# Performance work log

Measured on AMD Instinct MI355X. Metric: run time of the kernel, lower is better.

## Reference

```python
import jax, jax.numpy as jnp
import numpy as np

A = 32      # num_agents (nodes per batch element)
B = 256     # batch size
T = 5       # temporal_window_size
H, C = 4, 64  # attention heads, hidden_dim per head
D = H * C   # feature_dim = 256
NEG_SLOPE = 0.2
LATENT = 128
NBS = 64    # num_belief_states
FIN = NBS + 16  # node_feat_dim = num_belief_states + action_dim


def _xavier(k, shape):
    std = (2.0 / (shape[0] + shape[-1])) ** 0.5
    return std * jax.random.normal(k, shape, dtype=jnp.float32)


def setup_inputs() -> dict:
    key = jax.random.key(0)
    ks = jax.random.split(key, 24)
    N = B * A
    # fully-connected directed graph (no self loops) inside each batch block
    ii, jj = np.meshgrid(np.arange(A), np.arange(A), indexing='ij')
    m = ii != jj
    off = (np.arange(B) * A)[:, None]
    src = (off + ii[m][None, :]).ravel()
    dst = (off + jj[m][None, :]).ravel()
    edge_index = jnp.asarray(np.stack([src, dst]), dtype=jnp.int32)  # [2, E]
    return dict(
        x_seq=jax.random.normal(ks[0], (T, N, FIN), dtype=jnp.float32),
        edge_index=edge_index,
        W1=_xavier(ks[1], (D, FIN)),
        att_src1=0.1 * jax.random.normal(ks[2], (H, C), dtype=jnp.float32),
        att_dst1=0.1 * jax.random.normal(ks[3], (H, C), dtype=jnp.float32),
        b1=jnp.zeros((D,), jnp.float32),
        W2=_xavier(ks[4], (D, D)),
        att_src2=0.1 * jax.random.normal(ks[5], (H, C), dtype=jnp.float32),
        att_dst2=0.1 * jax.random.normal(ks[6], (H, C), dtype=jnp.float32),
        b2=jnp.zeros((D,), jnp.float32),
        in_proj_w=_xavier(ks[7], (3 * D, D)),
        in_proj_b=jnp.zeros((3 * D,), jnp.float32),
        out_proj_w=_xavier(ks[8], (D, D)),
        out_proj_b=jnp.zeros((D,), jnp.float32),
        w_mean=_xavier(ks[9], (LATENT, D)),
        b_mean=jnp.zeros((LATENT,), jnp.float32),
        w_logvar=_xavier(ks[10], (LATENT, D)),
        b_logvar=jnp.zeros((LATENT,), jnp.float32),
        w_belief=_xavier(ks[11], (NBS, D)),
        b_belief=jnp.zeros((NBS,), jnp.float32),
    )


def _gat(x, src, dst, W, a_src, a_dst, bias, N):
    """PyG-style GATConv (concat heads, self loops already in src/dst, eval mode)."""
    h = (x @ W.T).reshape(N, H, C)                         # [N,H,C]
    e = (h * a_src).sum(-1)[src] + (h * a_dst).sum(-1)[dst]  # [E,H]
    e = jax.nn.leaky_relu(e, NEG_SLOPE)
    mx = jax.ops.segment_max(e, dst, num_segments=N)       # segment softmax over incoming edges
    ex = jnp.exp(e - mx[dst])
    denom = jax.ops.segment_sum(ex, dst, num_segments=N)
    alpha = ex / denom[dst]                                # [E,H]
    out = jax.ops.segment_sum(h[src] * alpha[:, :, None], dst, num_segments=N)
    return out.reshape(N, H * C) + bias


def reference(x_seq, edge_index, W1, att_src1, att_dst1, b1, W2, att_src2, att_dst2, b2,
              in_proj_w, in_proj_b, out_proj_w, out_proj_b,
              w_mean, b_mean, w_logvar, b_logvar, w_belief, b_belief):
    N = x_seq.shape[1]
    loops = jnp.arange(N, dtype=edge_index.dtype)          # GATConv adds self loops
    src = jnp.concatenate([edge_index[0], loops])
    dst = jnp.concatenate([edge_index[1], loops])
    ego = jnp.arange(0, N, A)                              # ego node of each batch element

    def step(_, x):
        hh = jax.nn.relu(_gat(x, src, dst, W1, att_src1, att_dst1, b1, N))
        hh = jax.nn.relu(_gat(hh, src, dst, W2, att_src2, att_dst2, b2, N))
        return None, hh[ego]                               # [B, D]

    _, outs = jax.lax.scan(step, None, x_seq)              # [T, B, D]
    seq = jnp.transpose(outs, (1, 0, 2))                   # [B, T, D]

    # nn.MultiheadAttention(batch_first=True), float additive mask of 1s (j<=i) / 0s (j>i)
    qkv = seq @ in_proj_w.T + in_proj_b
    q, k, v = jnp.split(qkv, 3, axis=-1)
    split = lambda t: t.reshape(B, T, H, D // H).transpose(0, 2, 1, 3)  # [B,H,T,dh]
    q, k, v = split(q), split(k), split(v)
    mask = (jnp.arange(T)[:, None] >= jnp.arange(T)[None, :]).astype(seq.dtype)
    scale = 1.0 / jnp.sqrt(jnp.asarray(D // H, seq.dtype))
    scores = jnp.einsum('bhqd,bhkd->bhqk', q, k) * scale + mask
    attn = jax.nn.softmax(scores, axis=-1)
    ctx = jnp.einsum('bhqk,bhkd->bhqd', attn, v).transpose(0, 2, 1, 3).reshape(B, T, D)
    attn_out = ctx @ out_proj_w.T + out_proj_b
    feat = attn_out[:, -1]                                 # [B, D]

    mean = feat @ w_mean.T + b_mean
    logvar = feat @ w_logvar.T + b_logvar
    belief = jax.nn.softmax(feat @ w_belief.T + b_belief, axis=-1)
    return mean, logvar, belief
```

## Files before the change

### kernel.cpp

```cpp
#include <hip/hip_runtime.h>

typedef _Float16 f16;
typedef __attribute__((ext_vector_type(2))) _Float16 f16x2;
typedef __attribute__((ext_vector_type(4))) _Float16 f16x4;
typedef __attribute__((ext_vector_type(8))) _Float16 f16x8;
typedef __attribute__((ext_vector_type(4))) float    f32x4;

#define NA 32
#define NB 256
#define NT 5
#define ND 256
#define NFIN 80
#define NLAT 128
#define NBEL 64
#define NEG 0.2f

#define W1K 96
#define XSTR 104
#define H1TSTR 40
#define HH1STR 264
#define ALSTR 40

#define OFF_XS  0
#define OFF_ALP 6656
#define OFF_HH1 0
#define OFF_H1T 16896
#define OFF_SD  37376
#define SMEM_SZ 38400

#define MFMA16(a,b,c) __builtin_amdgcn_mfma_f32_16x16x32_f16(a, b, c, 0, 0, 0)

#define WS_SEQ   0
#define WS_QKV   655360
#define WS_Z2    655360
#define WS_CTX   2621440
#define WS_W1F   2752512
#define WS_W2F   2801664
#define WS_IPW   2932736
#define WS_OPW   3325952
#define WS_HDW   3457024
#define WS_WSD1  3620864
#define WS_WSD2  3623936

__global__ void convert_w(const float* __restrict__ W1, const float* __restrict__ W2,
                          const float* __restrict__ ipw, const float* __restrict__ opw,
                          const float* __restrict__ wm, const float* __restrict__ wl,
                          const float* __restrict__ wb,
                          const float* __restrict__ as1, const float* __restrict__ ad1,
                          const float* __restrict__ as2, const float* __restrict__ ad2,
                          f16* __restrict__ W1f, f16* __restrict__ W2f,
                          f16* __restrict__ ipwf, f16* __restrict__ opwf,
                          f16* __restrict__ hdwf,
                          f16* __restrict__ wsd1f, f16* __restrict__ wsd2f)
{
    const int i = blockIdx.x * 256 + threadIdx.x;
    if (i < 24576) {
        const int r = i / W1K, c = i - r * W1K;
        W1f[i] = (c < NFIN) ? (f16)W1[r * NFIN + c] : (f16)0.f;
    } else if (i < 90112) {
        const int j = i - 24576; W2f[j] = (f16)W2[j];
    } else if (i < 286720) {
        const int j = i - 90112; ipwf[j] = (f16)ipw[j];
    } else if (i < 352256) {
        const int j = i - 286720; opwf[j] = (f16)opw[j];
    } else if (i < 434176) {
        const int j = i - 352256;
        hdwf[j] = (f16)(j < 32768 ? wm[j] : (j < 65536 ? wl[j - 32768] : wb[j - 65536]));
    } else if (i < 435712) {
        const int j = i - 434176;
        const int o = j / 96, f = j - o * 96;
        float v = 0.f;
        if (o < 8 && f < NFIN) {
            const int h = o & 3;
            const float* av = (o < 4) ? as1 : ad1;
            for (int cc = 0; cc < 64; ++cc)
                v = fmaf(av[h * 64 + cc], W1[(h * 64 + cc) * NFIN + f], v);
        }
        wsd1f[j] = (f16)v;
    } else if (i < 439808) {
        const int j = i - 435712;
        const int o = j >> 8, k = j & 255;
        float v = 0.f;
        if (o < 8) {
            const int h = o & 3;
            const float* av = (o < 4) ? as2 : ad2;
            for (int cc = 0; cc < 64; ++cc)
                v = fmaf(av[h * 64 + cc], W2[(h * 64 + cc) * ND + k], v);
        }
        wsd2f[j] = (f16)v;
    }
}

__global__ __launch_bounds__(256, 2)
void gnn_kernel(const float* __restrict__ x_seq,
                const f16*  __restrict__ W1f,  const f16* __restrict__ wsd1f,
                const float* __restrict__ b1,
                const f16*  __restrict__ wsd2f,
                f16* __restrict__ z2g)
{
    __shared__ __align__(16) unsigned char smem[SMEM_SZ];
    f16*  Xs  = (f16*)(smem + OFF_XS);
    f16*  hh1 = (f16*)(smem + OFF_HH1);
    f16*  alp = (f16*)(smem + OFF_ALP);
    f16*  h1T = (f16*)(smem + OFF_H1T);
    float* sA = (float*)(smem + OFF_SD);
    float* dA = sA + 128;

    const int blk  = blockIdx.x;
    const int b    = blk / NT;
    const int t    = blk % NT;
    const int tid  = threadIdx.x;
    const int wv   = tid >> 6;
    const int lane = tid & 63;
    const int c    = lane & 15;
    const int g    = lane >> 4;
    const int n0   = wv * 64;
    const int kg   = 8 * g;

    f16x8 w1s[3], w1b[3][4];
#pragma unroll
    for (int kt = 0; kt < 3; ++kt) {
        const int k0 = kt * 32 + kg;
        w1s[kt] = *(const f16x8*)(wsd1f + c * W1K + k0);
#pragma unroll
        for (int tn = 0; tn < 4; ++tn)
            w1b[kt][tn] = *(const f16x8*)(W1f + (size_t)(n0 + 16 * tn + c) * W1K + k0);
    }

    const float* xg = x_seq + ((size_t)t * (NB * NA) + (size_t)b * NA) * NFIN;
    for (int idx = tid; idx < 640; idx += 256) {
        const int r = idx / 20, c4 = idx - r * 20;
        const float4 v = ((const float4*)xg)[idx];
        f16x4 h; h.x = (f16)v.x; h.y = (f16)v.y; h.z = (f16)v.z; h.w = (f16)v.w;
        *(f16x4*)(Xs + r * XSTR + c4 * 4) = h;
    }
    if (tid < 128) {
        const int r = tid >> 2, cc = tid & 3;
        f16x4 z; z.x = z.y = z.z = z.w = (f16)0.f;
        *(f16x4*)(Xs + r * XSTR + 80 + cc * 4) = z;
    }
    __syncthreads();

    f32x4 acc1[2][4]; f32x4 accS[2];
#pragma unroll
    for (int m = 0; m < 2; ++m) {
        accS[m] = (f32x4)0.f;
#pragma unroll
        for (int tn = 0; tn < 4; ++tn) acc1[m][tn] = (f32x4)0.f;
    }
#pragma unroll
    for (int kt = 0; kt < 3; ++kt) {
        const int k0 = kt * 32 + kg;
        f16x8 a0 = *(const f16x8*)(Xs + c * XSTR + k0);
        f16x8 a1 = *(const f16x8*)(Xs + (16 + c) * XSTR + k0);
        accS[0] = MFMA16(a0, w1s[kt], accS[0]);
        accS[1] = MFMA16(a1, w1s[kt], accS[1]);
#pragma unroll
        for (int tn = 0; tn < 4; ++tn) {
            acc1[0][tn] = MFMA16(a0, w1b[kt][tn], acc1[0][tn]);
            acc1[1][tn] = MFMA16(a1, w1b[kt][tn], acc1[1][tn]);
        }
    }

    if (c == wv) {
#pragma unroll
        for (int m = 0; m < 2; ++m)
#pragma unroll
            for (int r = 0; r < 4; ++r)
                sA[wv * 32 + 16 * m + 4 * g + r] = accS[m][r];
    } else if (c == wv + 4) {
#pragma unroll
        for (int m = 0; m < 2; ++m)
#pragma unroll
            for (int r = 0; r < 4; ++r)
                dA[wv * 32 + 16 * m + 4 * g + r] = accS[m][r];
    }

#pragma unroll
    for (int m = 0; m < 2; ++m)
#pragma unroll
        for (int tn = 0; tn < 4; ++tn) {
            f16x4 h;
            h.x = (f16)acc1[m][tn][0]; h.y = (f16)acc1[m][tn][1];
            h.z = (f16)acc1[m][tn][2]; h.w = (f16)acc1[m][tn][3];
            *(f16x4*)(h1T + (n0 + 16 * tn + c) * H1TSTR + 16 * m + 4 * g) = h;
        }

    {
        const int j = lane & 31;
        const int half = lane >> 5;
        const float dd = dA[wv * 32 + j];
        const float* sbase = sA + wv * 32 + 16 * half;
        float e[16]; float mx = -1e30f;
#pragma unroll
        for (int i = 0; i < 16; ++i) {
            float v = sbase[i] + dd;
            v = (v >= 0.f) ? v : NEG * v;
            e[i] = v; mx = fmaxf(mx, v);
        }
        mx = fmaxf(mx, __shfl_xor(mx, 32, 64));
        float den = 0.f;
#pragma unroll
        for (int i = 0; i < 16; ++i) { float p = __expf(e[i] - mx); e[i] = p; den += p; }
        den += __shfl_xor(den, 32, 64);
        const float rr = 1.f / den;
        f16* arow = alp + (wv * 32 + j) * ALSTR + 16 * half;
#pragma unroll
        for (int i2 = 0; i2 < 8; ++i2) {
            f16x2 p2; p2.x = (f16)(e[2 * i2] * rr); p2.y = (f16)(e[2 * i2 + 1] * rr);
            *(f16x2*)(arow + 2 * i2) = p2;
        }
    }

    f32x4 accT[4][2];
#pragma unroll
    for (int mt = 0; mt < 4; ++mt)
#pragma unroll
        for (int jt = 0; jt < 2; ++jt) accT[mt][jt] = (f32x4)0.f;
    {
        f16x8 bal0 = *(const f16x8*)(alp + (wv * 32 + c) * ALSTR + kg);
        f16x8 bal1 = *(const f16x8*)(alp + (wv * 32 + 16 + c) * ALSTR + kg);
#pragma unroll
        for (int mt = 0; mt < 4; ++mt) {
            f16x8 ah = *(const f16x8*)(h1T + (n0 + 16 * mt + c) * H1TSTR + kg);
            accT[mt][0] = MFMA16(ah, bal0, accT[mt][0]);
            accT[mt][1] = MFMA16(ah, bal1, accT[mt][1]);
        }
    }

    __syncthreads();

    f32x4 bqa[4];
#pragma unroll
    for (int mt = 0; mt < 4; ++mt)
        bqa[mt] = *(const f32x4*)&b1[n0 + 16 * mt + 4 * g];
#pragma unroll
    for (int mt = 0; mt < 4; ++mt) {
#pragma unroll
        for (int jt = 0; jt < 2; ++jt) {
            f16x4 h;
            h.x = (f16)fmaxf(accT[mt][jt][0] + bqa[mt][0], 0.f);
            h.y = (f16)fmaxf(accT[mt][jt][1] + bqa[mt][1], 0.f);
            h.z = (f16)fmaxf(accT[mt][jt][2] + bqa[mt][2], 0.f);
            h.w = (f16)fmaxf(accT[mt][jt][3] + bqa[mt][3], 0.f);
            *(f16x4*)(hh1 + (16 * jt + c) * HH1STR + n0 + 16 * mt + 4 * g) = h;
        }
    }
    __syncthreads();

    f16x8 w2s[8];
#pragma unroll
    for (int kt = 0; kt < 8; ++kt)
        w2s[kt] = *(const f16x8*)(wsd2f + c * ND + kt * 32 + kg);

    f32x4 accS2[2];
    accS2[0] = (f32x4)0.f; accS2[1] = (f32x4)0.f;
#pragma unroll
    for (int kt = 0; kt < 8; ++kt) {
        const int k0 = kt * 32 + kg;
        f16x8 a0 = *(const f16x8*)(hh1 + c * HH1STR + k0);
        f16x8 a1 = *(const f16x8*)(hh1 + (16 + c) * HH1STR + k0);
        accS2[0] = MFMA16(a0, w2s[kt], accS2[0]);
        accS2[1] = MFMA16(a1, w2s[kt], accS2[1]);
    }

    if (c == wv) {
#pragma unroll
        for (int m = 0; m < 2; ++m)
#pragma unroll
            for (int r = 0; r < 4; ++r)
                sA[wv * 32 + 16 * m + 4 * g + r] = accS2[m][r];
    }
    if (c == wv + 4 && g == 0) dA[wv * 32] = accS2[0][0];

    const float d20 = dA[wv * 32];

    {
        float mx = -1e30f;
#pragma unroll
        for (int i = 0; i < 32; ++i) {
            float v = sA[wv * 32 + i] + d20;
            v = (v >= 0.f) ? v : NEG * v;
            mx = fmaxf(mx, v);
        }
        float den = 0.f;
#pragma unroll
        for (int i = 0; i < 32; ++i) {
            float v = sA[wv * 32 + i] + d20;
            v = (v >= 0.f) ? v : NEG * v;
            den += __expf(v - mx);
        }
        float e0, e1;
        {
            float v = sA[wv * 32 + c] + d20;
            v = (v >= 0.f) ? v : NEG * v;
            e0 = __expf(v - mx);
        }
        {
            float v = sA[wv * 32 + 16 + c] + d20;
            v = (v >= 0.f) ? v : NEG * v;
            e1 = __expf(v - mx);
        }
        const float rden = 1.f / den;
        f16* zo = z2g + (size_t)blk * ND;
#pragma unroll
        for (int mt = 0; mt < 4; ++mt) {
            f32x4 zv;
#pragma unroll
            for (int r = 0; r < 4; ++r) {
                const float h0 = fmaxf(accT[mt][0][r] + bqa[mt][r], 0.f);
                const float h1v = fmaxf(accT[mt][1][r] + bqa[mt][r], 0.f);
                zv[r] = e0 * h0 + e1 * h1v;
            }
#pragma unroll
            for (int r = 0; r < 4; ++r) {
                zv[r] += __shfl_xor(zv[r], 1, 64);
                zv[r] += __shfl_xor(zv[r], 2, 64);
                zv[r] += __shfl_xor(zv[r], 4, 64);
                zv[r] += __shfl_xor(zv[r], 8, 64);
            }
            if (c == 0) {
                f16x4 h;
                h.x = (f16)(zv[0] * rden); h.y = (f16)(zv[1] * rden);
                h.z = (f16)(zv[2] * rden); h.w = (f16)(zv[3] * rden);
                *(f16x4*)(zo + n0 + 16 * mt + 4 * g) = h;
            }
        }
    }
}

#define QASTR 264
__global__ __launch_bounds__(256, 4)
void seq_kernel(const f16* __restrict__ z2g, const f16* __restrict__ W2f,
                const float* __restrict__ b2, f16* __restrict__ seqf)
{
    __shared__ __align__(16) f16 As[64 * QASTR];

    const int bx  = blockIdx.x;
    const int m0  = (bx % 20) * 64;
    const int n0  = (bx / 20) * 128;
    const int tid = threadIdx.x;
    const int wv  = tid >> 6;
    const int lane = tid & 63;
    const int c   = lane & 15;
    const int g   = lane >> 4;
    const int mb  = (wv >> 1) * 32;
    const int nb  = n0 + (wv & 1) * 64;

    for (int idx = tid; idx < 2048; idx += 256) {
        const int r = idx >> 5, c8 = idx & 31;
        *(f16x8*)(As + r * QASTR + c8 * 8) =
            *(const f16x8*)(z2g + (size_t)(m0 + r) * ND + c8 * 8);
    }
    __syncthreads();

    f32x4 acc[2][4];
#pragma unroll
    for (int m = 0; m < 2; ++m)
#pragma unroll
        for (int tn = 0; tn < 4; ++tn) acc[m][tn] = (f32x4)0.f;

#pragma unroll
    for (int kt = 0; kt < 8; ++kt) {
        const int k0 = kt * 32 + 8 * g;
        f16x8 a0 = *(const f16x8*)(As + (mb + c) * QASTR + k0);
        f16x8 a1 = *(const f16x8*)(As + (mb + 16 + c) * QASTR + k0);
#pragma unroll
        for (int tn = 0; tn < 4; ++tn) {
            f16x8 bw = *(const f16x8*)(W2f + (size_t)(nb + 16 * tn + c) * ND + k0);
            acc[0][tn] = MFMA16(a0, bw, acc[0][tn]);
            acc[1][tn] = MFMA16(a1, bw, acc[1][tn]);
        }
    }

    float bias[4];
#pragma unroll
    for (int tn = 0; tn < 4; ++tn) bias[tn] = b2[nb + 16 * tn + c];
#pragma unroll
    for (int m = 0; m < 2; ++m)
#pragma unroll
        for (int tn = 0; tn < 4; ++tn)
#pragma unroll
            for (int r = 0; r < 4; ++r) {
                const int row = m0 + mb + 16 * m + 4 * g + r;
                seqf[(size_t)row * ND + nb + 16 * tn + c] =
                    (f16)fmaxf(acc[m][tn][r] + bias[tn], 0.f);
            }
}

__global__ __launch_bounds__(256, 4)
void qkv_kernel(const f16* __restrict__ seqf, const f16* __restrict__ ipwf,
                const float* __restrict__ ipb, f16* __restrict__ qkv)
{
    __shared__ __align__(16) f16 As[64 * QASTR];

    const int bx  = blockIdx.x;
    const int m0  = (bx % 20) * 64;
    const int n0  = (bx / 20) * 128;
    const int tid = threadIdx.x;
    const int wv  = tid >> 6;
    const int lane = tid & 63;
    const int c   = lane & 15;
    const int g   = lane >> 4;
    const int mb  = (wv >> 1) * 32;
    const int nb  = n0 + (wv & 1) * 64;

    for (int idx = tid; idx < 2048; idx += 256) {
        const int r = idx >> 5, c8 = idx & 31;
        *(f16x8*)(As + r * QASTR + c8 * 8) =
            *(const f16x8*)(seqf + (size_t)(m0 + r) * ND + c8 * 8);
    }
    __syncthreads();

    f32x4 acc[2][4];
#pragma unroll
    for (int m = 0; m < 2; ++m)
#pragma unroll
        for (int tn = 0; tn < 4; ++tn) acc[m][tn] = (f32x4)0.f;

#pragma unroll
    for (int kt = 0; kt < 8; ++kt) {
        const int k0 = kt * 32 + 8 * g;
        f16x8 a0 = *(const f16x8*)(As + (mb + c) * QASTR + k0);
        f16x8 a1 = *(const f16x8*)(As + (mb + 16 + c) * QASTR + k0);
#pragma unroll
        for (int tn = 0; tn < 4; ++tn) {
            f16x8 bw = *(const f16x8*)(ipwf + (size_t)(nb + 16 * tn + c) * ND + k0);
            acc[0][tn] = MFMA16(a0, bw, acc[0][tn]);
            acc[1][tn] = MFMA16(a1, bw, acc[1][tn]);
        }
    }

    float bias[4];
#pragma unroll
    for (int tn = 0; tn < 4; ++tn) bias[tn] = ipb[nb + 16 * tn + c];
#pragma unroll
    for (int m = 0; m < 2; ++m)
#pragma unroll
        for (int tn = 0; tn < 4; ++tn)
#pragma unroll
            for (int r = 0; r < 4; ++r) {
                const int row = m0 + mb + 16 * m + 4 * g + r;
                qkv[(size_t)row * 768 + nb + 16 * tn + c] =
                    (f16)(acc[m][tn][r] + bias[tn]);
            }
}

__global__ __launch_bounds__(256, 4)
void attn_kernel(const f16* __restrict__ qkv, f16* __restrict__ ctx)
{
    const int b    = blockIdx.x;
    const int wv   = threadIdx.x >> 6;
    const int lane = threadIdx.x & 63;
    const int ch   = wv * 64 + lane;

    const float q = (float)qkv[(size_t)(b * 5 + 4) * 768 + ch];
    float kv[NT], vv[NT];
#pragma unroll
    for (int t = 0; t < NT; ++t) {
        kv[t] = (float)qkv[(size_t)(b * 5 + t) * 768 + 256 + ch];
        vv[t] = (float)qkv[(size_t)(b * 5 + t) * 768 + 512 + ch];
    }
    float sc[NT];
#pragma unroll
    for (int t = 0; t < NT; ++t) {
        float p = q * kv[t];
#pragma unroll
        for (int off = 32; off > 0; off >>= 1) p += __shfl_xor(p, off, 64);
        sc[t] = p * 0.125f;
    }
    float m = sc[0];
#pragma unroll
    for (int t = 1; t < NT; ++t) m = fmaxf(m, sc[t]);
    float den = 0.f, o = 0.f;
#pragma unroll
    for (int t = 0; t < NT; ++t) {
        float p = __expf(sc[t] - m);
        den += p;
        o = fmaf(p, vv[t], o);
    }
    ctx[(size_t)b * ND + ch] = (f16)(o / den);
}

#define FASTR 264
__global__ __launch_bounds__(256, 2)
void final_kernel(const f16* __restrict__ ctx,
                  const f16* __restrict__ opwf, const float* __restrict__ opb,
                  const f16* __restrict__ hdwf,
                  const float* __restrict__ bm, const float* __restrict__ blv,
                  const float* __restrict__ bb,
                  float* __restrict__ out)
{
    __shared__ __align__(16) f16 As[32 * FASTR];
    __shared__ __align__(16) f16 Fs[32 * FASTR];
    __shared__ __align__(16) float Bs[32 * 68];

    const int m0   = blockIdx.x * 32;
    const int tid  = threadIdx.x;
    const int wv   = tid >> 6;
    const int lane = tid & 63;
    const int c    = lane & 15;
    const int g    = lane >> 4;

    for (int idx = tid; idx < 1024; idx += 256) {
        const int r = idx >> 5, c8 = idx & 31;
        *(f16x8*)(As + r * FASTR + c8 * 8) =
            *(const f16x8*)(ctx + (size_t)(m0 + r) * ND + c8 * 8);
    }
    __syncthreads();

    {
        f32x4 acc[2][4];
#pragma unroll
        for (int m = 0; m < 2; ++m)
#pragma unroll
            for (int tn = 0; tn < 4; ++tn) acc[m][tn] = (f32x4)0.f;
#pragma unroll
        for (int kt = 0; kt < 8; ++kt) {
            const int k0 = kt * 32 + 8 * g;
            f16x8 a0 = *(const f16x8*)(As + c * FASTR + k0);
            f16x8 a1 = *(const f16x8*)(As + (16 + c) * FASTR + k0);
#pragma unroll
            for (int tn = 0; tn < 4; ++tn) {
                f16x8 bw = *(const f16x8*)(opwf + (size_t)(wv * 64 + 16 * tn + c) * ND + k0);
                acc[0][tn] = MFMA16(a0, bw, acc[0][tn]);
                acc[1][tn] = MFMA16(a1, bw, acc[1][tn]);
            }
        }
        float bias[4];
#pragma unroll
        for (int tn = 0; tn < 4; ++tn) bias[tn] = opb[wv * 64 + 16 * tn + c];
#pragma unroll
        for (int m = 0; m < 2; ++m)
#pragma unroll
            for (int tn = 0; tn < 4; ++tn)
#pragma unroll
                for (int r = 0; r < 4; ++r)
                    Fs[(16 * m + 4 * g + r) * FASTR + wv * 64 + 16 * tn + c] =
                        (f16)(acc[m][tn][r] + bias[tn]);
    }
    __syncthreads();

    {
        f32x4 acc[2][5];
#pragma unroll
        for (int m = 0; m < 2; ++m)
#pragma unroll
            for (int fi = 0; fi < 5; ++fi) acc[m][fi] = (f32x4)0.f;
#pragma unroll
        for (int kt = 0; kt < 8; ++kt) {
            const int k0 = kt * 32 + 8 * g;
            f16x8 a0 = *(const f16x8*)(Fs + c * FASTR + k0);
            f16x8 a1 = *(const f16x8*)(Fs + (16 + c) * FASTR + k0);
#pragma unroll
            for (int fi = 0; fi < 5; ++fi) {
                const int nf = 5 * wv + fi;
                f16x8 bw = *(const f16x8*)(hdwf + (size_t)(16 * nf + c) * ND + k0);
                acc[0][fi] = MFMA16(a0, bw, acc[0][fi]);
                acc[1][fi] = MFMA16(a1, bw, acc[1][fi]);
            }
        }
#pragma unroll
        for (int fi = 0; fi < 5; ++fi) {
            const int ocol = 16 * (5 * wv + fi) + c;
            float bias;
            if (ocol < 128)       bias = bm[ocol];
            else if (ocol < 256)  bias = blv[ocol - 128];
            else                  bias = bb[ocol - 256];
#pragma unroll
            for (int m = 0; m < 2; ++m)
#pragma unroll
                for (int r = 0; r < 4; ++r) {
                    const int row = 16 * m + 4 * g + r;
                    const float v = acc[m][fi][r] + bias;
                    if (ocol < 128)
                        out[(size_t)(m0 + row) * NLAT + ocol] = v;
                    else if (ocol < 256)
                        out[(size_t)NB * NLAT + (size_t)(m0 + row) * NLAT + (ocol - 128)] = v;
                    else
                        Bs[row * 68 + (ocol - 256)] = v;
                }
        }
    }
    __syncthreads();

    for (int rr = 0; rr < 8; ++rr) {
        const int row = wv * 8 + rr;
        float x = Bs[row * 68 + lane];
        float mm = x;
#pragma unroll
        for (int off = 32; off > 0; off >>= 1) mm = fmaxf(mm, __shfl_xor(mm, off, 64));
        float p = __expf(x - mm);
        float dd = p;
#pragma unroll
        for (int off = 32; off > 0; off >>= 1) dd += __shfl_xor(dd, off, 64);
        out[(size_t)2 * NB * NLAT + (size_t)(m0 + row) * NBEL + lane] = p / dd;
    }
}

extern "C" void kernel_launch(void* const* d_in, const int* in_sizes, int n_in,
                              void* d_out, int out_size, void* d_ws, size_t ws_size,
                              hipStream_t stream)
{
    (void)in_sizes; (void)n_in; (void)out_size; (void)ws_size;
    const float* x_seq = (const float*)d_in[0];
    const float* W1  = (const float*)d_in[2];
    const float* as1 = (const float*)d_in[3];
    const float* ad1 = (const float*)d_in[4];
    const float* b1  = (const float*)d_in[5];
    const float* W2  = (const float*)d_in[6];
    const float* as2 = (const float*)d_in[7];
    const float* ad2 = (const float*)d_in[8];
    const float* b2  = (const float*)d_in[9];
    const float* ipw = (const float*)d_in[10];
    const float* ipb = (const float*)d_in[11];
    const float* opw = (const float*)d_in[12];
    const float* opb = (const float*)d_in[13];
    const float* wm  = (const float*)d_in[14];
    const float* bm  = (const float*)d_in[15];
    const float* wl  = (const float*)d_in[16];
    const float* bl  = (const float*)d_in[17];
    const float* wb  = (const float*)d_in[18];
    const float* bb  = (const float*)d_in[19];

    char* ws = (char*)d_ws;
    f16* seqf  = (f16*)(ws + WS_SEQ);
    f16* qkv   = (f16*)(ws + WS_QKV);
    f16* z2g   = (f16*)(ws + WS_Z2);
    f16* ctx   = (f16*)(ws + WS_CTX);
    f16* W1f   = (f16*)(ws + WS_W1F);
    f16* W2f   = (f16*)(ws + WS_W2F);
    f16* ipwf  = (f16*)(ws + WS_IPW);
    f16* opwf  = (f16*)(ws + WS_OPW);
    f16* hdwf  = (f16*)(ws + WS_HDW);
    f16* wsd1f = (f16*)(ws + WS_WSD1);
    f16* wsd2f = (f16*)(ws + WS_WSD2);
    float* out = (float*)d_out;

    hipLaunchKernelGGL(convert_w, dim3(1718), dim3(256), 0, stream,
                       W1, W2, ipw, opw, wm, wl, wb, as1, ad1, as2, ad2,
                       W1f, W2f, ipwf, opwf, hdwf, wsd1f, wsd2f);
    hipLaunchKernelGGL(gnn_kernel, dim3(NB * NT), dim3(256), 0, stream,
                       x_seq, W1f, wsd1f, b1, wsd2f, z2g);
    hipLaunchKernelGGL(seq_kernel, dim3(40), dim3(256), 0, stream,
                       z2g, W2f, b2, seqf);
    hipLaunchKernelGGL(qkv_kernel, dim3(120), dim3(256), 0, stream,
                       seqf, ipwf, ipb, qkv);
    hipLaunchKernelGGL(attn_kernel, dim3(NB), dim3(256), 0, stream, qkv, ctx);
    hipLaunchKernelGGL(final_kernel, dim3(8), dim3(256), 0, stream,
                       ctx, opwf, opb, hdwf, bm, bl, bb, out);
}
```

Before: 62.16 us.

## Fuse seq+QKV projections and attention+output heads into two kernels

Merges the W2 projection and QKV in-projection into one kernel that keeps the ReLU'd sequence tile in shared memory. It also merges attention, out-projection and the mean/logvar/belief heads into one kernel that processes 16 batch rows per block with vectorized loads. This removes two kernel launches and the global round trips for seqf and ctx. In exchange each block does more serial work: 40 blocks each compute all 768 QKV columns and only 16 blocks run the tail, so parallelism drops and per-block latency rises.

```diff
diff --git a/kernel.cpp b/kernel.cpp
--- a/kernel.cpp
+++ b/kernel.cpp
@@ -30,10 +30,7 @@
 
 #define MFMA16(a,b,c) __builtin_amdgcn_mfma_f32_16x16x32_f16(a, b, c, 0, 0, 0)
 
-#define WS_SEQ   0
 #define WS_QKV   655360
-#define WS_Z2    655360
-#define WS_CTX   2621440
 #define WS_W1F   2752512
 #define WS_W2F   2801664
 #define WS_IPW   2932736
@@ -41,6 +38,7 @@
 #define WS_HDW   3457024
 #define WS_WSD1  3620864
 #define WS_WSD2  3623936
+#define WS_Z2    4194304
 
 __global__ void convert_w(const float* __restrict__ W1, const float* __restrict__ W2,
                           const float* __restrict__ ipw, const float* __restrict__ opw,
@@ -329,171 +327,15 @@
     }
 }
 
-#define QASTR 264
-__global__ __launch_bounds__(256, 4)
-void seq_kernel(const f16* __restrict__ z2g, const f16* __restrict__ W2f,
-                const float* __restrict__ b2, f16* __restrict__ seqf)
+#define TSTR 264
+__global__ __launch_bounds__(256, 2)
+void seqqkv_kernel(const f16* __restrict__ z2g, const f16* __restrict__ W2f,
+                   const float* __restrict__ b2,
+                   const f16* __restrict__ ipwf, const float* __restrict__ ipb,
+                   f16* __restrict__ qkv)
 {
-    __shared__ __align__(16) f16 As[64 * QASTR];
-
-    const int bx  = blockIdx.x;
-    const int m0  = (bx % 20) * 64;
-    const int n0  = (bx / 20) * 128;
-    const int tid = threadIdx.x;
-    const int wv  = tid >> 6;
-    const int lane = tid & 63;
-    const int c   = lane & 15;
-    const int g   = lane >> 4;
-    const int mb  = (wv >> 1) * 32;
-    const int nb  = n0 + (wv & 1) * 64;
-
-    for (int idx = tid; idx < 2048; idx += 256) {
-        const int r = idx >> 5, c8 = idx & 31;
-        *(f16x8*)(As + r * QASTR + c8 * 8) =
-            *(const f16x8*)(z2g + (size_t)(m0 + r) * ND + c8 * 8);
-    }
-    __syncthreads();
-
-    f32x4 acc[2][4];
-#pragma unroll
-    for (int m = 0; m < 2; ++m)
-#pragma unroll
-        for (int tn = 0; tn < 4; ++tn) acc[m][tn] = (f32x4)0.f;
-
-#pragma unroll
-    for (int kt = 0; kt < 8; ++kt) {
-        const int k0 = kt * 32 + 8 * g;
-        f16x8 a0 = *(const f16x8*)(As + (mb + c) * QASTR + k0);
-        f16x8 a1 = *(const f16x8*)(As + (mb + 16 + c) * QASTR + k0);
-#pragma unroll
-        for (int tn = 0; tn < 4; ++tn) {
-            f16x8 bw = *(const f16x8*)(W2f + (size_t)(nb + 16 * tn + c) * ND + k0);
-            acc[0][tn] = MFMA16(a0, bw, acc[0][tn]);
-            acc[1][tn] = MFMA16(a1, bw, acc[1][tn]);
-        }
-    }
-
-    float bias[4];
-#pragma unroll
-    for (int tn = 0; tn < 4; ++tn) bias[tn] = b2[nb + 16 * tn + c];
-#pragma unroll
-    for (int m = 0; m < 2; ++m)
-#pragma unroll
-        for (int tn = 0; tn < 4; ++tn)
-#pragma unroll
-            for (int r = 0; r < 4; ++r) {
-                const int row = m0 + mb + 16 * m + 4 * g + r;
-                seqf[(size_t)row * ND + nb + 16 * tn + c] =
-                    (f16)fmaxf(acc[m][tn][r] + bias[tn], 0.f);
-            }
-}
-
-__global__ __launch_bounds__(256, 4)
-void qkv_kernel(const f16* __restrict__ seqf, const f16* __restrict__ ipwf,
-                const float* __restrict__ ipb, f16* __restrict__ qkv)
-{
-    __shared__ __align__(16) f16 As[64 * QASTR];
-
-    const int bx  = blockIdx.x;
-    const int m0  = (bx % 20) * 64;
-    const int n0  = (bx / 20) * 128;
-    const int tid = threadIdx.x;
-    const int wv  = tid >> 6;
-    const int lane = tid & 63;
-    const int c   = lane & 15;
-    const int g   = lane >> 4;
-    const int mb  = (wv >> 1) * 32;
-    const int nb  = n0 + (wv & 1) * 64;
-
-    for (int idx = tid; idx < 2048; idx += 256) {
-        const int r = idx >> 5, c8 = idx & 31;
-        *(f16x8*)(As + r * QASTR + c8 * 8) =
-            *(const f16x8*)(seqf + (size_t)(m0 + r) * ND + c8 * 8);
-    }
-    __syncthreads();
-
-    f32x4 acc[2][4];
-#pragma unroll
-    for (int m = 0; m < 2; ++m)
-#pragma unroll
-        for (int tn = 0; tn < 4; ++tn) acc[m][tn] = (f32x4)0.f;
-
-#pragma unroll
-    for (int kt = 0; kt < 8; ++kt) {
-        const int k0 = kt * 32 + 8 * g;
-        f16x8 a0 = *(const f16x8*)(As + (mb + c) * QASTR + k0);
-        f16x8 a1 = *(const f16x8*)(As + (mb + 16 + c) * QASTR + k0);
-#pragma unroll
-        for (int tn = 0; tn < 4; ++tn) {
-            f16x8 bw = *(const f16x8*)(ipwf + (size_t)(nb + 16 * tn + c) * ND + k0);
-            acc[0][tn] = MFMA16(a0, bw, acc[0][tn]);
-            acc[1][tn] = MFMA16(a1, bw, acc[1][tn]);
-        }
-    }
-
-    float bias[4];
-#pragma unroll
-    for (int tn = 0; tn < 4; ++tn) bias[tn] = ipb[nb + 16 * tn + c];
-#pragma unroll
-    for (int m = 0; m < 2; ++m)
-#pragma unroll
-        for (int tn = 0; tn < 4; ++tn)
-#pragma unroll
-            for (int r = 0; r < 4; ++r) {
-                const int row = m0 + mb + 16 * m + 4 * g + r;
-                qkv[(size_t)row * 768 + nb + 16 * tn + c] =
-                    (f16)(acc[m][tn][r] + bias[tn]);
-            }
-}
-
-__global__ __launch_bounds__(256, 4)
-void attn_kernel(const f16* __restrict__ qkv, f16* __restrict__ ctx)
-{
-    const int b    = blockIdx.x;
-    const int wv   = threadIdx.x >> 6;
-    const int lane = threadIdx.x & 63;
-    const int ch   = wv * 64 + lane;
-
-    const float q = (float)qkv[(size_t)(b * 5 + 4) * 768 + ch];
-    float kv[NT], vv[NT];
-#pragma unroll
-    for (int t = 0; t < NT; ++t) {
-        kv[t] = (float)qkv[(size_t)(b * 5 + t) * 768 + 256 + ch];
-        vv[t] = (float)qkv[(size_t)(b * 5 + t) * 768 + 512 + ch];
-    }
-    float sc[NT];
-#pragma unroll
-    for (int t = 0; t < NT; ++t) {
-        float p = q * kv[t];
-#pragma unroll
-        for (int off = 32; off > 0; off >>= 1) p += __shfl_xor(p, off, 64);
-        sc[t] = p * 0.125f;
-    }
-    float m = sc[0];
-#pragma unroll
-    for (int t = 1; t < NT; ++t) m = fmaxf(m, sc[t]);
-    float den = 0.f, o = 0.f;
-#pragma unroll
-    for (int t = 0; t < NT; ++t) {
-        float p = __expf(sc[t] - m);
-        den += p;
-        o = fmaf(p, vv[t], o);
-    }
-    ctx[(size_t)b * ND + ch] = (f16)(o / den);
-}
-
-#define FASTR 264
-__global__ __launch_bounds__(256, 2)
-void final_kernel(const f16* __restrict__ ctx,
-                  const f16* __restrict__ opwf, const float* __restrict__ opb,
-                  const f16* __restrict__ hdwf,
-                  const float* __restrict__ bm, const float* __restrict__ blv,
-                  const float* __restrict__ bb,
-                  float* __restrict__ out)
-{
-    __shared__ __align__(16) f16 As[32 * FASTR];
-    __shared__ __align__(16) f16 Fs[32 * FASTR];
-    __shared__ __align__(16) float Bs[32 * 68];
+    __shared__ __align__(16) f16 As[32 * TSTR];
+    __shared__ __align__(16) f16 Ss[32 * TSTR];
 
     const int m0   = blockIdx.x * 32;
     const int tid  = threadIdx.x;
@@ -501,15 +343,53 @@
     const int lane = tid & 63;
     const int c    = lane & 15;
     const int g    = lane >> 4;
+    const int kg   = 8 * g;
+    const int n0   = wv * 64;
 
     for (int idx = tid; idx < 1024; idx += 256) {
         const int r = idx >> 5, c8 = idx & 31;
-        *(f16x8*)(As + r * FASTR + c8 * 8) =
-            *(const f16x8*)(ctx + (size_t)(m0 + r) * ND + c8 * 8);
+        *(f16x8*)(As + r * TSTR + c8 * 8) =
+            *(const f16x8*)(z2g + (size_t)(m0 + r) * ND + c8 * 8);
     }
     __syncthreads();
 
     {
+        f32x4 acc[4][2];
+#pragma unroll
+        for (int tn = 0; tn < 4; ++tn)
+#pragma unroll
+            for (int jt = 0; jt < 2; ++jt) acc[tn][jt] = (f32x4)0.f;
+#pragma unroll
+        for (int kt = 0; kt < 8; ++kt) {
+            const int k0 = kt * 32 + kg;
+            f16x8 bz0 = *(const f16x8*)(As + c * TSTR + k0);
+            f16x8 bz1 = *(const f16x8*)(As + (16 + c) * TSTR + k0);
+#pragma unroll
+            for (int tn = 0; tn < 4; ++tn) {
+                f16x8 aw = *(const f16x8*)(W2f + (size_t)(n0 + 16 * tn + c) * ND + k0);
+                acc[tn][0] = MFMA16(aw, bz0, acc[tn][0]);
+                acc[tn][1] = MFMA16(aw, bz1, acc[tn][1]);
+            }
+        }
+#pragma unroll
+        for (int tn = 0; tn < 4; ++tn) {
+            const float4 bq = *(const float4*)&b2[n0 + 16 * tn + 4 * g];
+#pragma unroll
+            for (int jt = 0; jt < 2; ++jt) {
+                f16x4 h;
+                h.x = (f16)fmaxf(acc[tn][jt][0] + bq.x, 0.f);
+                h.y = (f16)fmaxf(acc[tn][jt][1] + bq.y, 0.f);
+                h.z = (f16)fmaxf(acc[tn][jt][2] + bq.z, 0.f);
+                h.w = (f16)fmaxf(acc[tn][jt][3] + bq.w, 0.f);
+                *(f16x4*)(Ss + (16 * jt + c) * TSTR + n0 + 16 * tn + 4 * g) = h;
+            }
+        }
+    }
+    __syncthreads();
+
+#pragma unroll
+    for (int ch = 0; ch < 3; ++ch) {
+        const int ncol = ch * 256 + n0;
         f32x4 acc[2][4];
 #pragma unroll
         for (int m = 0; m < 2; ++m)
@@ -517,75 +397,176 @@
             for (int tn = 0; tn < 4; ++tn) acc[m][tn] = (f32x4)0.f;
 #pragma unroll
         for (int kt = 0; kt < 8; ++kt) {
-            const int k0 = kt * 32 + 8 * g;
-            f16x8 a0 = *(const f16x8*)(As + c * FASTR + k0);
-            f16x8 a1 = *(const f16x8*)(As + (16 + c) * FASTR + k0);
+            const int k0 = kt * 32 + kg;
+            f16x8 a0 = *(const f16x8*)(Ss + c * TSTR + k0);
+            f16x8 a1 = *(const f16x8*)(Ss + (16 + c) * TSTR + k0);
 #pragma unroll
             for (int tn = 0; tn < 4; ++tn) {
-                f16x8 bw = *(const f16x8*)(opwf + (size_t)(wv * 64 + 16 * tn + c) * ND + k0);
+                f16x8 bw = *(const f16x8*)(ipwf + (size_t)(ncol + 16 * tn + c) * ND + k0);
                 acc[0][tn] = MFMA16(a0, bw, acc[0][tn]);
                 acc[1][tn] = MFMA16(a1, bw, acc[1][tn]);
             }
         }
-        float bias[4];
-#pragma unroll
-        for (int tn = 0; tn < 4; ++tn) bias[tn] = opb[wv * 64 + 16 * tn + c];
-#pragma unroll
-        for (int m = 0; m < 2; ++m)
-#pragma unroll
-            for (int tn = 0; tn < 4; ++tn)
-#pragma unroll
-                for (int r = 0; r < 4; ++r)
-                    Fs[(16 * m + 4 * g + r) * FASTR + wv * 64 + 16 * tn + c] =
-                        (f16)(acc[m][tn][r] + bias[tn]);
-    }
-    __syncthreads();
+#pragma unroll
+        for (int tn = 0; tn < 4; ++tn) {
+            const float bias = ipb[ncol + 16 * tn + c];
+#pragma unroll
+            for (int m = 0; m < 2; ++m)
+#pragma unroll
+                for (int r = 0; r < 4; ++r) {
+                    const int row = m0 + 16 * m + 4 * g + r;
+                    qkv[(size_t)row * 768 + ncol + 16 * tn + c] =
+                        (f16)(acc[m][tn][r] + bias);
+                }
+        }
+    }
+}
+
+__global__ __launch_bounds__(256, 2)
+void attnfinal_kernel(const f16* __restrict__ qkv,
+                      const f16* __restrict__ opwf, const float* __restrict__ opb,
+                      const f16* __restrict__ hdwf,
+                      const float* __restrict__ bm, const float* __restrict__ blv,
+                      const float* __restrict__ bb,
+                      float* __restrict__ out)
+{
+    __shared__ __align__(16) f16 ctx[16 * TSTR];
+    __shared__ __align__(16) f16 Fs[16 * TSTR];
+    __shared__ __align__(16) float Bs[16 * 68];
+
+    const int bb0  = blockIdx.x * 16;
+    const int tid  = threadIdx.x;
+    const int wv   = tid >> 6;
+    const int lane = tid & 63;
+    const int c    = lane & 15;
+    const int g    = lane >> 4;
+    const int kg   = 8 * g;
 
     {
-        f32x4 acc[2][5];
-#pragma unroll
-        for (int m = 0; m < 2; ++m)
-#pragma unroll
-            for (int fi = 0; fi < 5; ++fi) acc[m][fi] = (f32x4)0.f;
+        const int bq = lane >> 2;
+        const int q4 = lane & 3;
+        const int chb = wv * 64 + 16 * q4;
+        const size_t rowq = (size_t)(bb0 + bq) * 5 + 4;
+
+        f16x8 q0 = *(const f16x8*)(qkv + rowq * 768 + chb);
+        f16x8 q1 = *(const f16x8*)(qkv + rowq * 768 + chb + 8);
+        f16x8 k0a[NT], k1a[NT], v0a[NT], v1a[NT];
+#pragma unroll
+        for (int t = 0; t < NT; ++t) {
+            const size_t rt = (size_t)(bb0 + bq) * 5 + t;
+            k0a[t] = *(const f16x8*)(qkv + rt * 768 + 256 + chb);
+            k1a[t] = *(const f16x8*)(qkv + rt * 768 + 256 + chb + 8);
+            v0a[t] = *(const f16x8*)(qkv + rt * 768 + 512 + chb);
+            v1a[t] = *(const f16x8*)(qkv + rt * 768 + 512 + chb + 8);
+        }
+        float sc[NT];
+#pragma unroll
+        for (int t = 0; t < NT; ++t) {
+            float s = 0.f;
+#pragma unroll
+            for (int i = 0; i < 8; ++i) {
+                s = fmaf((float)q0[i], (float)k0a[t][i], s);
+                s = fmaf((float)q1[i], (float)k1a[t][i], s);
+            }
+            s += __shfl_xor(s, 1, 64);
+            s += __shfl_xor(s, 2, 64);
+            sc[t] = s * 0.125f;
+        }
+        float mx = sc[0];
+#pragma unroll
+        for (int t = 1; t < NT; ++t) mx = fmaxf(mx, sc[t]);
+        float den = 0.f;
+        float cacc[16];
+#pragma unroll
+        for (int i = 0; i < 16; ++i) cacc[i] = 0.f;
+#pragma unroll
+        for (int t = 0; t < NT; ++t) {
+            const float p = __expf(sc[t] - mx);
+            den += p;
+#pragma unroll
+            for (int i = 0; i < 8; ++i) {
+                cacc[i]     = fmaf(p, (float)v0a[t][i], cacc[i]);
+                cacc[i + 8] = fmaf(p, (float)v1a[t][i], cacc[i + 8]);
+            }
+        }
+        const float rden = 1.f / den;
+        f16x8 h0, h1;
+#pragma unroll
+        for (int i = 0; i < 8; ++i) {
+            h0[i] = (f16)(cacc[i] * rden);
+            h1[i] = (f16)(cacc[i + 8] * rden);
+        }
+        *(f16x8*)(ctx + bq * TSTR + chb) = h0;
+        *(f16x8*)(ctx + bq * TSTR + chb + 8) = h1;
+    }
+    __syncthreads();
+
+    {
+        const int n0 = wv * 64;
+        f32x4 acc[4];
+#pragma unroll
+        for (int tn = 0; tn < 4; ++tn) acc[tn] = (f32x4)0.f;
 #pragma unroll
         for (int kt = 0; kt < 8; ++kt) {
-            const int k0 = kt * 32 + 8 * g;
-            f16x8 a0 = *(const f16x8*)(Fs + c * FASTR + k0);
-            f16x8 a1 = *(const f16x8*)(Fs + (16 + c) * FASTR + k0);
+            const int k0 = kt * 32 + kg;
+            f16x8 bc = *(const f16x8*)(ctx + c * TSTR + k0);
+#pragma unroll
+            for (int tn = 0; tn < 4; ++tn) {
+                f16x8 aw = *(const f16x8*)(opwf + (size_t)(n0 + 16 * tn + c) * ND + k0);
+                acc[tn] = MFMA16(aw, bc, acc[tn]);
+            }
+        }
+#pragma unroll
+        for (int tn = 0; tn < 4; ++tn) {
+            const float4 bq = *(const float4*)&opb[n0 + 16 * tn + 4 * g];
+            f16x4 h;
+            h.x = (f16)(acc[tn][0] + bq.x);
+            h.y = (f16)(acc[tn][1] + bq.y);
+            h.z = (f16)(acc[tn][2] + bq.z);
+            h.w = (f16)(acc[tn][3] + bq.w);
+            *(f16x4*)(Fs + c * TSTR + n0 + 16 * tn + 4 * g) = h;
+        }
+    }
+    __syncthreads();
+
+    {
+        f32x4 acc[5];
+#pragma unroll
+        for (int fi = 0; fi < 5; ++fi) acc[fi] = (f32x4)0.f;
+#pragma unroll
+        for (int kt = 0; kt < 8; ++kt) {
+            const int k0 = kt * 32 + kg;
+            f16x8 bf = *(const f16x8*)(Fs + c * TSTR + k0);
 #pragma unroll
             for (int fi = 0; fi < 5; ++fi) {
                 const int nf = 5 * wv + fi;
-                f16x8 bw = *(const f16x8*)(hdwf + (size_t)(16 * nf + c) * ND + k0);
-                acc[0][fi] = MFMA16(a0, bw, acc[0][fi]);
-                acc[1][fi] = MFMA16(a1, bw, acc[1][fi]);
+                f16x8 aw = *(const f16x8*)(hdwf + (size_t)(16 * nf + c) * ND + k0);
+                acc[fi] = MFMA16(aw, bf, acc[fi]);
             }
         }
 #pragma unroll
         for (int fi = 0; fi < 5; ++fi) {
-            const int ocol = 16 * (5 * wv + fi) + c;
-            float bias;
-            if (ocol < 128)       bias = bm[ocol];
-            else if (ocol < 256)  bias = blv[ocol - 128];
-            else                  bias = bb[ocol - 256];
-#pragma unroll
-            for (int m = 0; m < 2; ++m)
-#pragma unroll
-                for (int r = 0; r < 4; ++r) {
-                    const int row = 16 * m + 4 * g + r;
-                    const float v = acc[m][fi][r] + bias;
-                    if (ocol < 128)
-                        out[(size_t)(m0 + row) * NLAT + ocol] = v;
-                    else if (ocol < 256)
-                        out[(size_t)NB * NLAT + (size_t)(m0 + row) * NLAT + (ocol - 128)] = v;
-                    else
-                        Bs[row * 68 + (ocol - 256)] = v;
-                }
-        }
-    }
-    __syncthreads();
-
-    for (int rr = 0; rr < 8; ++rr) {
-        const int row = wv * 8 + rr;
+            const int ocol = 16 * (5 * wv + fi) + 4 * g;
+            float4 bias;
+            if (ocol < 128)       bias = *(const float4*)&bm[ocol];
+            else if (ocol < 256)  bias = *(const float4*)&blv[ocol - 128];
+            else                  bias = *(const float4*)&bb[ocol - 256];
+            float4 v;
+            v.x = acc[fi][0] + bias.x; v.y = acc[fi][1] + bias.y;
+            v.z = acc[fi][2] + bias.z; v.w = acc[fi][3] + bias.w;
+            if (ocol < 128)
+                *(float4*)&out[(size_t)(bb0 + c) * NLAT + ocol] = v;
+            else if (ocol < 256)
+                *(float4*)&out[(size_t)NB * NLAT + (size_t)(bb0 + c) * NLAT + (ocol - 128)] = v;
+            else
+                *(float4*)&Bs[c * 68 + (ocol - 256)] = v;
+        }
+    }
+    __syncthreads();
+
+#pragma unroll
+    for (int rr = 0; rr < 4; ++rr) {
+        const int row = wv * 4 + rr;
         float x = Bs[row * 68 + lane];
         float mm = x;
 #pragma unroll
@@ -594,7 +575,7 @@
         float dd = p;
 #pragma unroll
         for (int off = 32; off > 0; off >>= 1) dd += __shfl_xor(dd, off, 64);
-        out[(size_t)2 * NB * NLAT + (size_t)(m0 + row) * NBEL + lane] = p / dd;
+        out[(size_t)2 * NB * NLAT + (size_t)(bb0 + row) * NBEL + lane] = p / dd;
     }
 }
 
@@ -624,10 +605,8 @@
     const float* bb  = (const float*)d_in[19];
 
     char* ws = (char*)d_ws;
-    f16* seqf  = (f16*)(ws + WS_SEQ);
     f16* qkv   = (f16*)(ws + WS_QKV);
     f16* z2g   = (f16*)(ws + WS_Z2);
-    f16* ctx   = (f16*)(ws + WS_CTX);
     f16* W1f   = (f16*)(ws + WS_W1F);
     f16* W2f   = (f16*)(ws + WS_W2F);
     f16* ipwf  = (f16*)(ws + WS_IPW);
@@ -642,11 +621,8 @@
                        W1f, W2f, ipwf, opwf, hdwf, wsd1f, wsd2f);
     hipLaunchKernelGGL(gnn_kernel, dim3(NB * NT), dim3(256), 0, stream,
                        x_seq, W1f, wsd1f, b1, wsd2f, z2g);
-    hipLaunchKernelGGL(seq_kernel, dim3(40), dim3(256), 0, stream,
-                       z2g, W2f, b2, seqf);
-    hipLaunchKernelGGL(qkv_kernel, dim3(120), dim3(256), 0, stream,
-                       seqf, ipwf, ipb, qkv);
-    hipLaunchKernelGGL(attn_kernel, dim3(NB), dim3(256), 0, stream, qkv, ctx);
-    hipLaunchKernelGGL(final_kernel, dim3(8), dim3(256), 0, stream,
-                       ctx, opwf, opb, hdwf, bm, bl, bb, out);
+    hipLaunchKernelGGL(seqqkv_kernel, dim3(40), dim3(256), 0, stream,
+                       z2g, W2f, b2, ipwf, ipb, qkv);
+    hipLaunchKernelGGL(attnfinal_kernel, dim3(16), dim3(256), 0, stream,
+                       qkv, opwf, opb, hdwf, bm, bl, bb, out);
 }
```

After: 68.87 us. +10.8%, slower.
